# Performance work log

Measured on AMD Instinct MI355X. Metric: run time of the kernel, lower is better.

Reference implementation:

```python
import jax, jax.numpy as jnp
import numpy as np

N_NODES = 100000
N_EDGES = 1000000
IN_FEATS = 64
HID = 128
NUM_CLASSES = 10


def setup_inputs() -> dict:
    key = jax.random.key(0)
    ks = jax.random.split(key, 8)
    x = jax.random.normal(ks[0], (N_NODES, IN_FEATS), dtype=jnp.float32)
    edge_index = jax.random.randint(ks[1], (2, N_EDGES), 0, N_NODES, dtype=jnp.int64)
    # Glorot-style init scale for weights
    def w(k, fan_in, fan_out):
        s = (2.0 / (fan_in + fan_out)) ** 0.5
        return jax.random.normal(k, (fan_in, fan_out), dtype=jnp.float32) * s
    return {
        "x": x,
        "edge_index": edge_index,
        "W1": w(ks[2], IN_FEATS, HID),
        "b1": jnp.zeros((HID,), dtype=jnp.float32),
        "W2": w(ks[3], HID, HID),
        "b2": jnp.zeros((HID,), dtype=jnp.float32),
        "Wl": w(ks[4], HID, NUM_CLASSES),
        "bl": jnp.zeros((NUM_CLASSES,), dtype=jnp.float32),
    }


def _gcn_conv(x, src, dst, norm, W, b, num_nodes):
    # PyG GCNConv: h = x W, then out_i = sum_{j->i} norm_ij * h_j + b
    h = x @ W  # [N, out]
    msgs = h[src] * norm[:, None]  # gather + scale  [E+N, out]
    out = jax.ops.segment_sum(msgs, dst, num_segments=num_nodes)
    return out + b


def reference(x, edge_index, W1, b1, W2, b2, Wl, bl):
    N = x.shape[0]
    loops = jnp.arange(N, dtype=edge_index.dtype)
    src = jnp.concatenate([edge_index[0], loops])  # source nodes (messages from)
    dst = jnp.concatenate([edge_index[1], loops])  # target nodes (aggregate at)
    # symmetric normalization: deg over targets (includes self-loops)
    deg = jax.ops.segment_sum(jnp.ones(dst.shape, dtype=x.dtype), dst, num_segments=N)
    dinv = jnp.where(deg > 0, jax.lax.rsqrt(deg), 0.0)
    norm = dinv[src] * dinv[dst]  # [E+N]

    h = jax.nn.relu(_gcn_conv(x, src, dst, norm, W1, b1, N))
    h = jax.nn.relu(_gcn_conv(h, src, dst, norm, W2, b2, N))
    return jax.nn.log_softmax(h @ Wl + bl, axis=1)
```

## Files before the change

kernel.cpp:

```cpp
#include <hip/hip_runtime.h>
#include <hip/hip_fp16.h>
#include <math.h>

#define NUM_CLASSES 10

#define BSH 7
#define BSZ 128
#define BCAP 1792
#define NBMAX 1024
#define P1BATCH 4096

typedef _Float16 half8  __attribute__((ext_vector_type(8)));
typedef _Float16 half4t __attribute__((ext_vector_type(4)));
typedef float    floatx4 __attribute__((ext_vector_type(4)));

__global__ __launch_bounds__(256) void prep_kernel(const float* __restrict__ W1,
                                                   const float* __restrict__ W2,
                                                   const float* __restrict__ Wlc,
                                                   _Float16* __restrict__ W1t,
                                                   _Float16* __restrict__ W2t,
                                                   _Float16* __restrict__ Wct,
                                                   int* __restrict__ fill, int nbuck) {
    const int b = blockIdx.x, tid = threadIdx.x;
    if (b == 0) {
        for (int i = tid; i < nbuck; i += 256) fill[i] = 0;
    }
    if (b < 32) {
        int i = b * 256 + tid;
        int k = i >> 7, c = i & 127;
        W1t[c * 72 + k] = (_Float16)W1[i];
    } else if (b < 96) {
        int i = (b - 32) * 256 + tid;
        int k = i >> 7, c = i & 127;
        W2t[c * 136 + k] = (_Float16)W2[i];
    } else {
        for (int i = tid; i < 16 * 136; i += 256) {
            int c = i / 136, k = i - c * 136;
            float v = (c < NUM_CLASSES && k < 128) ? Wlc[k * NUM_CLASSES + c] : 0.0f;
            Wct[i] = (_Float16)v;
        }
    }
}

__global__ __launch_bounds__(256) void csr_p1_kernel(const int* __restrict__ src,
                                                     const int* __restrict__ dst,
                                                     int* __restrict__ bucket_fill,
                                                     unsigned* __restrict__ pairs, int E) {
    __shared__ int hist[NBMAX], base[NBMAX], cur[NBMAX];
    const int tid = threadIdx.x;
    for (int i = tid; i < NBMAX; i += 256) { hist[i] = 0; cur[i] = 0; }
    __syncthreads();
    const int bb = blockIdx.x * P1BATCH;
    unsigned pk[16];
    int bk[16];
    int cnt = 0;
#pragma unroll
    for (int i = 0; i < 16; ++i) {
        int idx = bb + i * 256 + tid;
        if (idx < E) {
            int s = src[idx], d = dst[idx];
            bk[i] = d >> BSH;
            pk[i] = ((unsigned)s << BSH) | (unsigned)(d & (BSZ - 1));
            atomicAdd(&hist[bk[i]], 1);
            cnt = i + 1;
        }
    }
    __syncthreads();
    for (int i = tid; i < NBMAX; i += 256)
        if (hist[i] > 0) base[i] = atomicAdd(&bucket_fill[i], hist[i]);
    __syncthreads();
#pragma unroll
    for (int i = 0; i < 16; ++i) {
        if (i < cnt) {
            int b = bk[i];
            int r = atomicAdd(&cur[b], 1) + base[b];
            if (r < BCAP) pairs[(size_t)b * BCAP + r] = pk[i];
        }
    }
}

__global__ __launch_bounds__(256) void scan_base_kernel(const int* __restrict__ fill,
                                                        int* __restrict__ bbase, int nbuck) {
    __shared__ int s1[256];
    const int tid = threadIdx.x;
    const int i0 = tid * 4;
    int v[4];
#pragma unroll
    for (int j = 0; j < 4; ++j) v[j] = (i0 + j < nbuck) ? fill[i0 + j] : 0;
    int t = v[0] + v[1] + v[2] + v[3];
    s1[tid] = t;
    __syncthreads();
    for (int off = 1; off < 256; off <<= 1) {
        int u = (tid >= off) ? s1[tid - off] : 0;
        __syncthreads();
        s1[tid] += u;
        __syncthreads();
    }
    int run = s1[tid] - t;
#pragma unroll
    for (int j = 0; j < 4; ++j) {
        if (i0 + j < nbuck) { bbase[i0 + j] = run; run += v[j]; }
    }
    if (tid == 255) bbase[nbuck] = s1[255];
}

__global__ __launch_bounds__(256) void csr_p2_kernel(const int* __restrict__ bucket_fill,
                                                     const int* __restrict__ bucket_base,
                                                     const unsigned* __restrict__ pairs,
                                                     const float* __restrict__ x,
                                                     int* __restrict__ rowstart,
                                                     float* __restrict__ dinv,
                                                     int* __restrict__ csr_src,
                                                     __half2* __restrict__ xs_h,
                                                     int N, int nbuck) {
    __shared__ int cnt[BSZ], excl[BSZ], cur[BSZ];
    __shared__ int s1[BSZ];
    const int tid = threadIdx.x;
    const int b = blockIdx.x;
    const int node0 = b << BSH;
    const int nodes_b = min(BSZ, N - node0);

    if (tid < BSZ) { cnt[tid] = 0; cur[tid] = 0; }
    __syncthreads();
    const int bbase = bucket_base[b];
    const int ne = bucket_fill[b];

    const unsigned* bp = pairs + (size_t)b * BCAP;
    for (int i = tid; i < ne; i += 256)
        atomicAdd(&cnt[bp[i] & (BSZ - 1)], 1);
    __syncthreads();
    int c = (tid < BSZ) ? cnt[tid] : 0;
    if (tid < BSZ) s1[tid] = c;
    __syncthreads();
    for (int off = 1; off < BSZ; off <<= 1) {
        int t = (tid < BSZ && tid >= off) ? s1[tid - off] : 0;
        __syncthreads();
        if (tid < BSZ) s1[tid] += t;
        __syncthreads();
    }
    if (tid < BSZ) excl[tid] = s1[tid] - c;
    __syncthreads();

    if (tid < nodes_b) {
        rowstart[node0 + tid] = bbase + excl[tid];
        dinv[node0 + tid] = rsqrtf((float)cnt[tid] + 1.0f);
    }
    if (b == nbuck - 1 && tid == 0) rowstart[N] = bbase + ne;

    for (int i = tid; i < nodes_b * 32; i += 256) {
        int ln = i >> 5;
        float d = rsqrtf((float)cnt[ln] + 1.0f);
        float2 v = ((const float2*)x)[(size_t)node0 * 32 + i];
        xs_h[(size_t)node0 * 32 + i] = __floats2half2_rn(v.x * d, v.y * d);
    }
    for (int i = tid; i < ne; i += 256) {
        unsigned p = bp[i];
        int d = (int)(p & (BSZ - 1));
        int r = atomicAdd(&cur[d], 1);
        csr_src[bbase + excl[d] + r] = (int)(p >> BSH);
    }
}

template <int F>
__global__ __launch_bounds__(256) void gather_h_kernel(const __half2* __restrict__ hs,
                                                       const float* __restrict__ dinv,
                                                       const int* __restrict__ rowstart,
                                                       const int* __restrict__ csr_src,
                                                       __half2* __restrict__ out, int N) {
    constexpr int F2 = F / 2;
    int node = (blockIdx.x * 256 + threadIdx.x) >> 6;
    int lane = threadIdx.x & 63;
    if (node >= N) return;
    int f2 = lane & (F2 - 1);

    int beg = rowstart[node];
    int end = rowstart[node + 1];
    int deg = end - beg;

    float2 self = __half22float2(hs[(size_t)node * F2 + f2]);
    float2 acc;

    if (deg <= 16) {
        int myidx = (lane < deg) ? csr_src[beg + lane] : node;
        float comp = (float)(deg - 15);
        acc.x = self.x * comp;
        acc.y = self.y * comp;
        float2 v[16];
#pragma unroll
        for (int u = 0; u < 16; ++u) {
            int s = __shfl(myidx, u);
            v[u] = __half22float2(hs[(size_t)s * F2 + f2]);
        }
#pragma unroll
        for (int u = 0; u < 16; ++u) { acc.x += v[u].x; acc.y += v[u].y; }
    } else {
        int lim = deg < 64 ? deg : 64;
        int myidx = (lane < lim) ? csr_src[beg + lane] : node;
        int itersUp = (lim + 7) & ~7;
        float comp = (float)(1 - (itersUp - lim));
        acc.x = self.x * comp;
        acc.y = self.y * comp;
        for (int j = 0; j < itersUp; j += 8) {
            int s[8];
#pragma unroll
            for (int u = 0; u < 8; ++u) s[u] = __shfl(myidx, j + u);
            float2 v[8];
#pragma unroll
            for (int u = 0; u < 8; ++u) v[u] = __half22float2(hs[(size_t)s[u] * F2 + f2]);
#pragma unroll
            for (int u = 0; u < 8; ++u) { acc.x += v[u].x; acc.y += v[u].y; }
        }
        for (int j = beg + 64; j < end; ++j) {
            int s = csr_src[j];
            float2 v = __half22float2(hs[(size_t)s * F2 + f2]);
            acc.x += v.x;
            acc.y += v.y;
        }
    }

    if (F == 128 || lane < 32) {
        float d = dinv[node];
        out[(size_t)node * F2 + f2] = __floats2half2_rn(d * acc.x, d * acc.y);
    }
}

template <int K, bool SCALE_OUT>
__global__ __launch_bounds__(256) void gemm_mfma_kernel(const _Float16* __restrict__ In,
                                                        const _Float16* __restrict__ Wt,
                                                        const float* __restrict__ bias,
                                                        const float* __restrict__ dinv,
                                                        _Float16* __restrict__ Out, int N) {
    constexpr int KP = K + 8;
    constexpr int NC = K / 32;
    __shared__ _Float16 Wl[128 * KP];
    __shared__ float bias_s[128];
    const int tid = threadIdx.x;

    for (int i = tid; i < (128 * KP) / 8; i += 256)
        ((floatx4*)Wl)[i] = ((const floatx4*)Wt)[i];
    if (tid < 128) bias_s[tid] = bias[tid];
    __syncthreads();

    const int lane = tid & 63;
    const int wave = tid >> 6;
    const int q = lane >> 4;
    const int l15 = lane & 15;

#pragma unroll
    for (int iter = 0; iter < 2; ++iter) {
        int myrow = blockIdx.x * 128 + iter * 64 + wave * 16 + l15;
        int r = myrow < N ? myrow : N - 1;
        half8 xf[NC];
#pragma unroll
        for (int c = 0; c < NC; ++c)
            xf[c] = *(const half8*)(In + (size_t)r * K + c * 32 + q * 8);
        floatx4 acc[8];
#pragma unroll
        for (int t = 0; t < 8; ++t) acc[t] = (floatx4){0.f, 0.f, 0.f, 0.f};
#pragma unroll
        for (int c = 0; c < NC; ++c) {
#pragma unroll
            for (int t = 0; t < 8; ++t) {
                half8 wf = *(const half8*)(Wl + (t * 16 + l15) * KP + c * 32 + q * 8);
                acc[t] = __builtin_amdgcn_mfma_f32_16x16x32_f16(wf, xf[c], acc[t], 0, 0, 0);
            }
        }
        if (myrow < N) {
            float sc = SCALE_OUT ? dinv[myrow] : 1.0f;
#pragma unroll
            for (int t = 0; t < 8; ++t) {
                int c0 = t * 16 + q * 4;
                floatx4 bv = *(const floatx4*)&bias_s[c0];
                half4t h;
#pragma unroll
                for (int j = 0; j < 4; ++j)
                    h[j] = (_Float16)(sc * fmaxf(acc[t][j] + bv[j], 0.0f));
                *(half4t*)(Out + (size_t)myrow * 128 + c0) = h;
            }
        }
    }
}

__global__ __launch_bounds__(256) void gemm_final_kernel(const _Float16* __restrict__ In,
                                                         const _Float16* __restrict__ Wt,
                                                         const float* __restrict__ bias,
                                                         const _Float16* __restrict__ Wct,
                                                         const float* __restrict__ bl,
                                                         float* __restrict__ out, int N) {
    constexpr int K = 128, KP = 136, NC = 4;
    __shared__ _Float16 Wl[128 * KP];
    __shared__ _Float16 Wc[16 * KP];
    __shared__ float bias_s[128];
    __shared__ float bl_s[16];
    __shared__ _Float16 act_s[4][16 * KP];
    const int tid = threadIdx.x;

    for (int i = tid; i < (128 * KP) / 8; i += 256)
        ((floatx4*)Wl)[i] = ((const floatx4*)Wt)[i];
    for (int i = tid; i < (16 * KP) / 8; i += 256)
        ((floatx4*)Wc)[i] = ((const floatx4*)Wct)[i];
    if (tid < 128) bias_s[tid] = bias[tid];
    if (tid < 16) bl_s[tid] = (tid < NUM_CLASSES) ? bl[tid] : -1e30f;
    __syncthreads();

    const int lane = tid & 63;
    const int wave = tid >> 6;
    const int q = lane >> 4;
    const int l15 = lane & 15;
    _Float16* As = act_s[wave];

    half8 wcf[NC];
#pragma unroll
    for (int c = 0; c < NC; ++c)
        wcf[c] = *(const half8*)(Wc + l15 * KP + c * 32 + q * 8);
    float myclsb[4];
#pragma unroll
    for (int reg = 0; reg < 4; ++reg) myclsb[reg] = bl_s[q * 4 + reg];

#pragma unroll
    for (int iter = 0; iter < 2; ++iter) {
        int rowbase = blockIdx.x * 128 + iter * 64 + wave * 16;
        int myrow = rowbase + l15;
        int r = myrow < N ? myrow : N - 1;
        half8 xf[NC];
#pragma unroll
        for (int c = 0; c < NC; ++c)
            xf[c] = *(const half8*)(In + (size_t)r * K + c * 32 + q * 8);
        floatx4 acc[8];
#pragma unroll
        for (int t = 0; t < 8; ++t) acc[t] = (floatx4){0.f, 0.f, 0.f, 0.f};
#pragma unroll
        for (int c = 0; c < NC; ++c) {
#pragma unroll
            for (int t = 0; t < 8; ++t) {
                half8 wf = *(const half8*)(Wl + (t * 16 + l15) * KP + c * 32 + q * 8);
                acc[t] = __builtin_amdgcn_mfma_f32_16x16x32_f16(wf, xf[c], acc[t], 0, 0, 0);
            }
        }
#pragma unroll
        for (int t = 0; t < 8; ++t) {
            int c0 = t * 16 + q * 4;
            floatx4 bv = *(const floatx4*)&bias_s[c0];
            half4t h;
#pragma unroll
            for (int j = 0; j < 4; ++j)
                h[j] = (_Float16)fmaxf(acc[t][j] + bv[j], 0.0f);
            *(half4t*)&As[l15 * KP + c0] = h;
        }
        floatx4 lg = (floatx4){0.f, 0.f, 0.f, 0.f};
#pragma unroll
        for (int c = 0; c < NC; ++c) {
            half8 af = *(const half8*)(As + l15 * KP + c * 32 + q * 8);
            lg = __builtin_amdgcn_mfma_f32_16x16x32_f16(wcf[c], af, lg, 0, 0, 0);
        }
        if (myrow < N) {
            float v[4];
#pragma unroll
            for (int reg = 0; reg < 4; ++reg) v[reg] = lg[reg] + myclsb[reg];
            float mx = fmaxf(fmaxf(v[0], v[1]), fmaxf(v[2], v[3]));
            mx = fmaxf(mx, __shfl_xor(mx, 16));
            mx = fmaxf(mx, __shfl_xor(mx, 32));
            float sm = expf(v[0] - mx) + expf(v[1] - mx) + expf(v[2] - mx) + expf(v[3] - mx);
            sm += __shfl_xor(sm, 16);
            sm += __shfl_xor(sm, 32);
            float lse = mx + logf(sm);
#pragma unroll
            for (int reg = 0; reg < 4; ++reg) {
                int cls = q * 4 + reg;
                if (cls < NUM_CLASSES)
                    out[(size_t)myrow * NUM_CLASSES + cls] = v[reg] - lse;
            }
        }
    }
}

extern "C" void kernel_launch(void* const* d_in, const int* in_sizes, int n_in,
                              void* d_out, int out_size, void* d_ws, size_t ws_size,
                              hipStream_t stream) {
    const float* x  = (const float*)d_in[0];
    const int*   ei = (const int*)d_in[1];
    const float* W1 = (const float*)d_in[2];
    const float* b1 = (const float*)d_in[3];
    const float* W2 = (const float*)d_in[4];
    const float* b2 = (const float*)d_in[5];
    const float* Wlc = (const float*)d_in[6];
    const float* bl = (const float*)d_in[7];
    float* out = (float*)d_out;

    const int N = in_sizes[0] / 64;
    const int E = in_sizes[1] / 2;
    const int* src = ei;
    const int* dst = ei + E;
    const int nbuck = (N + BSZ - 1) >> BSH;

    char* ws = (char*)d_ws;
    int*      bucket_fill = (int*)(ws + 0);
    int*      rowstart    = (int*)(ws + 4096);
    float*    dinv        = (float*)(ws + 524288);
    _Float16* W1t         = (_Float16*)(ws + 1048576);
    _Float16* W2t         = (_Float16*)(ws + 1069056);
    _Float16* Wct         = (_Float16*)(ws + 1103872);
    int*      bucket_base = (int*)(ws + 1110016);
    unsigned* pairs       = (unsigned*)(ws + 2097152);
    int*      csr_src     = (int*)(ws + 12582912);
    char*     region1     = ws + 16777216;
    char*     region2     = ws + 68157440;
    __half2*  xs_h = (__half2*)region1;
    __half2*  g1h  = (__half2*)(region1 + 13631488);
    __half2*  g2h  = (__half2*)region1;
    __half2*  a1_h = (__half2*)region2;

    const int P1B = (E + P1BATCH - 1) / P1BATCH;
    const int GB  = (N + 127) / 128;
    const int WVB = (N + 3) / 4;

    prep_kernel<<<97, 256, 0, stream>>>(W1, W2, Wlc, W1t, W2t, Wct, bucket_fill, nbuck);
    csr_p1_kernel<<<P1B, 256, 0, stream>>>(src, dst, bucket_fill, pairs, E);
    scan_base_kernel<<<1, 256, 0, stream>>>(bucket_fill, bucket_base, nbuck);
    csr_p2_kernel<<<nbuck, 256, 0, stream>>>(bucket_fill, bucket_base, pairs, x, rowstart,
                                             dinv, csr_src, xs_h, N, nbuck);

    gather_h_kernel<64><<<WVB, 256, 0, stream>>>(xs_h, dinv, rowstart, csr_src, g1h, N);
    gemm_mfma_kernel<64, true><<<GB, 256, 0, stream>>>((const _Float16*)g1h, W1t, b1, dinv,
                                                       (_Float16*)a1_h, N);

    gather_h_kernel<128><<<WVB, 256, 0, stream>>>(a1_h, dinv, rowstart, csr_src, g2h, N);
    gemm_final_kernel<<<GB, 256, 0, stream>>>((const _Float16*)g2h, W2t, b2, Wct, bl, out, N);
}
```

Measured before the change: 226.0 us.

## Fuse prep into CSR pass, drop scan kernel, split gathers by feature width

Merges the weight-conversion prep kernel into the CSR bucketing pass and zeroes the bucket counts with an async memset. The first pass now stages its pairs in shared memory, sorted by bucket, so the global writes come out contiguous. The separate single-block scan kernel is removed, and each csr_p2 block instead reduces the preceding bucket counts itself. The 64-feature gather now uses both half-waves, each taking alternate neighbours, and combines the two halves with a cross-lane shuffle. Together these aim to cut launch count and idle lanes, at the cost of redundant prefix sums in every p2 block and more shared memory per block in the first pass.

Result: slower. 233.0 us (+3.1%).

```diff
diff --git a/kernel.cpp b/kernel.cpp
--- a/kernel.cpp
+++ b/kernel.cpp
@@ -9,48 +9,57 @@
 #define BCAP 1792
 #define NBMAX 1024
 #define P1BATCH 4096
+#define PREPB 97
 
 typedef _Float16 half8  __attribute__((ext_vector_type(8)));
 typedef _Float16 half4t __attribute__((ext_vector_type(4)));
 typedef float    floatx4 __attribute__((ext_vector_type(4)));
 
-__global__ __launch_bounds__(256) void prep_kernel(const float* __restrict__ W1,
-                                                   const float* __restrict__ W2,
-                                                   const float* __restrict__ Wlc,
-                                                   _Float16* __restrict__ W1t,
-                                                   _Float16* __restrict__ W2t,
-                                                   _Float16* __restrict__ Wct,
-                                                   int* __restrict__ fill, int nbuck) {
-    const int b = blockIdx.x, tid = threadIdx.x;
-    if (b == 0) {
-        for (int i = tid; i < nbuck; i += 256) fill[i] = 0;
-    }
-    if (b < 32) {
-        int i = b * 256 + tid;
-        int k = i >> 7, c = i & 127;
-        W1t[c * 72 + k] = (_Float16)W1[i];
-    } else if (b < 96) {
-        int i = (b - 32) * 256 + tid;
-        int k = i >> 7, c = i & 127;
-        W2t[c * 136 + k] = (_Float16)W2[i];
-    } else {
-        for (int i = tid; i < 16 * 136; i += 256) {
-            int c = i / 136, k = i - c * 136;
-            float v = (c < NUM_CLASSES && k < 128) ? Wlc[k * NUM_CLASSES + c] : 0.0f;
-            Wct[i] = (_Float16)v;
-        }
-    }
-}
-
-__global__ __launch_bounds__(256) void csr_p1_kernel(const int* __restrict__ src,
-                                                     const int* __restrict__ dst,
-                                                     int* __restrict__ bucket_fill,
-                                                     unsigned* __restrict__ pairs, int E) {
-    __shared__ int hist[NBMAX], base[NBMAX], cur[NBMAX];
+__global__ __launch_bounds__(256) void prep_p1_kernel(const float* __restrict__ W1,
+                                                      const float* __restrict__ W2,
+                                                      const float* __restrict__ Wlc,
+                                                      _Float16* __restrict__ W1t,
+                                                      _Float16* __restrict__ W2t,
+                                                      _Float16* __restrict__ Wct,
+                                                      const int* __restrict__ src,
+                                                      const int* __restrict__ dst,
+                                                      int* __restrict__ bucket_fill,
+                                                      unsigned* __restrict__ pairs, int E) {
+    __shared__ int hist[NBMAX];
+    __shared__ int lofs[NBMAX];
+    __shared__ int gbase[NBMAX];
+    __shared__ int cur[NBMAX];
+    __shared__ int s1[256];
+    __shared__ unsigned stage[P1BATCH];
+    __shared__ unsigned short sbk[P1BATCH];
     const int tid = threadIdx.x;
+    const int b = blockIdx.x;
+
+    if (b < PREPB) {
+        if (b < 32) {
+            int i = b * 256 + tid;
+            int k = i >> 7, c = i & 127;
+            W1t[c * 72 + k] = (_Float16)W1[i];
+        } else if (b < 96) {
+            int i = (b - 32) * 256 + tid;
+            int k = i >> 7, c = i & 127;
+            W2t[c * 136 + k] = (_Float16)W2[i];
+        } else {
+            for (int i = tid; i < 16 * 136; i += 256) {
+                int c = i / 136, k = i - c * 136;
+                float v = (c < NUM_CLASSES && k < 128) ? Wlc[k * NUM_CLASSES + c] : 0.0f;
+                Wct[i] = (_Float16)v;
+            }
+        }
+        return;
+    }
+
+    const int blk = b - PREPB;
     for (int i = tid; i < NBMAX; i += 256) { hist[i] = 0; cur[i] = 0; }
     __syncthreads();
-    const int bb = blockIdx.x * P1BATCH;
+
+    const int bb = blk * P1BATCH;
+    const int bcnt = min(P1BATCH, E - bb);
     unsigned pk[16];
     int bk[16];
     int cnt = 0;
@@ -66,46 +75,45 @@
         }
     }
     __syncthreads();
-    for (int i = tid; i < NBMAX; i += 256)
-        if (hist[i] > 0) base[i] = atomicAdd(&bucket_fill[i], hist[i]);
+    const int i0 = tid * 4;
+    int h4[4];
+    int ssum = 0;
+#pragma unroll
+    for (int j = 0; j < 4; ++j) { h4[j] = hist[i0 + j]; ssum += h4[j]; }
+    s1[tid] = ssum;
+    __syncthreads();
+    for (int off = 1; off < 256; off <<= 1) {
+        int t = (tid >= off) ? s1[tid - off] : 0;
+        __syncthreads();
+        s1[tid] += t;
+        __syncthreads();
+    }
+    int run = s1[tid] - ssum;
+#pragma unroll
+    for (int j = 0; j < 4; ++j) { lofs[i0 + j] = run; run += h4[j]; }
+#pragma unroll
+    for (int j = 0; j < 4; ++j)
+        gbase[i0 + j] = (h4[j] > 0) ? atomicAdd(&bucket_fill[i0 + j], h4[j]) : 0;
     __syncthreads();
 #pragma unroll
     for (int i = 0; i < 16; ++i) {
         if (i < cnt) {
-            int b = bk[i];
-            int r = atomicAdd(&cur[b], 1) + base[b];
-            if (r < BCAP) pairs[(size_t)b * BCAP + r] = pk[i];
-        }
-    }
-}
-
-__global__ __launch_bounds__(256) void scan_base_kernel(const int* __restrict__ fill,
-                                                        int* __restrict__ bbase, int nbuck) {
-    __shared__ int s1[256];
-    const int tid = threadIdx.x;
-    const int i0 = tid * 4;
-    int v[4];
-#pragma unroll
-    for (int j = 0; j < 4; ++j) v[j] = (i0 + j < nbuck) ? fill[i0 + j] : 0;
-    int t = v[0] + v[1] + v[2] + v[3];
-    s1[tid] = t;
-    __syncthreads();
-    for (int off = 1; off < 256; off <<= 1) {
-        int u = (tid >= off) ? s1[tid - off] : 0;
-        __syncthreads();
-        s1[tid] += u;
-        __syncthreads();
-    }
-    int run = s1[tid] - t;
-#pragma unroll
-    for (int j = 0; j < 4; ++j) {
-        if (i0 + j < nbuck) { bbase[i0 + j] = run; run += v[j]; }
-    }
-    if (tid == 255) bbase[nbuck] = s1[255];
+            int bi = bk[i];
+            int r = atomicAdd(&cur[bi], 1);
+            int slot = lofs[bi] + r;
+            stage[slot] = pk[i];
+            sbk[slot] = (unsigned short)bi;
+        }
+    }
+    __syncthreads();
+    for (int j = tid; j < bcnt; j += 256) {
+        int bi = sbk[j];
+        int g = gbase[bi] + (j - lofs[bi]);
+        if (g < BCAP) pairs[(size_t)bi * BCAP + g] = stage[j];
+    }
 }
 
 __global__ __launch_bounds__(256) void csr_p2_kernel(const int* __restrict__ bucket_fill,
-                                                     const int* __restrict__ bucket_base,
                                                      const unsigned* __restrict__ pairs,
                                                      const float* __restrict__ x,
                                                      int* __restrict__ rowstart,
@@ -114,16 +122,24 @@
                                                      __half2* __restrict__ xs_h,
                                                      int N, int nbuck) {
     __shared__ int cnt[BSZ], excl[BSZ], cur[BSZ];
-    __shared__ int s1[BSZ];
+    __shared__ int s1[256];
     const int tid = threadIdx.x;
     const int b = blockIdx.x;
     const int node0 = b << BSH;
     const int nodes_b = min(BSZ, N - node0);
 
     if (tid < BSZ) { cnt[tid] = 0; cur[tid] = 0; }
-    __syncthreads();
-    const int bbase = bucket_base[b];
+    int part = 0;
+    for (int j = tid; j < b; j += 256) part += bucket_fill[j];
+    s1[tid] = part;
+    __syncthreads();
+    for (int off = 128; off > 0; off >>= 1) {
+        if (tid < off) s1[tid] += s1[tid + off];
+        __syncthreads();
+    }
+    const int bbase = s1[0];
     const int ne = bucket_fill[b];
+    __syncthreads();
 
     const unsigned* bp = pairs + (size_t)b * BCAP;
     for (int i = tid; i < ne; i += 256)
@@ -161,67 +177,113 @@
     }
 }
 
-template <int F>
-__global__ __launch_bounds__(256) void gather_h_kernel(const __half2* __restrict__ hs,
+__global__ __launch_bounds__(256) void gather64_kernel(const __half2* __restrict__ xs,
                                                        const float* __restrict__ dinv,
                                                        const int* __restrict__ rowstart,
                                                        const int* __restrict__ csr_src,
                                                        __half2* __restrict__ out, int N) {
-    constexpr int F2 = F / 2;
     int node = (blockIdx.x * 256 + threadIdx.x) >> 6;
     int lane = threadIdx.x & 63;
     if (node >= N) return;
-    int f2 = lane & (F2 - 1);
+    const int h = lane >> 5;
+    const int f2 = lane & 31;
 
     int beg = rowstart[node];
     int end = rowstart[node + 1];
     int deg = end - beg;
 
-    float2 self = __half22float2(hs[(size_t)node * F2 + f2]);
-    float2 acc;
+    float2 self = __half22float2(xs[(size_t)node * 32 + f2]);
+    float2 acc = make_float2(0.f, 0.f);
 
     if (deg <= 16) {
         int myidx = (lane < deg) ? csr_src[beg + lane] : node;
-        float comp = (float)(deg - 15);
-        acc.x = self.x * comp;
-        acc.y = self.y * comp;
-        float2 v[16];
-#pragma unroll
-        for (int u = 0; u < 16; ++u) {
-            int s = __shfl(myidx, u);
-            v[u] = __half22float2(hs[(size_t)s * F2 + f2]);
-        }
-#pragma unroll
-        for (int u = 0; u < 16; ++u) { acc.x += v[u].x; acc.y += v[u].y; }
+        if (h == 0) {
+            float cmp = (float)(deg - 15);
+            acc.x = self.x * cmp;
+            acc.y = self.y * cmp;
+        }
+        float2 v[8];
+#pragma unroll
+        for (int u = 0; u < 8; ++u) {
+            int s = __shfl(myidx, 2 * u + h);
+            v[u] = __half22float2(xs[(size_t)s * 32 + f2]);
+        }
+#pragma unroll
+        for (int u = 0; u < 8; ++u) { acc.x += v[u].x; acc.y += v[u].y; }
     } else {
         int lim = deg < 64 ? deg : 64;
         int myidx = (lane < lim) ? csr_src[beg + lane] : node;
-        int itersUp = (lim + 7) & ~7;
-        float comp = (float)(1 - (itersUp - lim));
-        acc.x = self.x * comp;
-        acc.y = self.y * comp;
-        for (int j = 0; j < itersUp; j += 8) {
-            int s[8];
-#pragma unroll
-            for (int u = 0; u < 8; ++u) s[u] = __shfl(myidx, j + u);
+        int itersUp = (lim + 15) & ~15;
+        if (h == 0) {
+            float cmp = (float)(1 - (itersUp - lim));
+            acc.x = self.x * cmp;
+            acc.y = self.y * cmp;
+        }
+        for (int j = 0; j < itersUp; j += 16) {
             float2 v[8];
 #pragma unroll
-            for (int u = 0; u < 8; ++u) v[u] = __half22float2(hs[(size_t)s[u] * F2 + f2]);
+            for (int u = 0; u < 8; ++u) {
+                int s = __shfl(myidx, j + 2 * u + h);
+                v[u] = __half22float2(xs[(size_t)s * 32 + f2]);
+            }
 #pragma unroll
             for (int u = 0; u < 8; ++u) { acc.x += v[u].x; acc.y += v[u].y; }
         }
-        for (int j = beg + 64; j < end; ++j) {
-            int s = csr_src[j];
-            float2 v = __half22float2(hs[(size_t)s * F2 + f2]);
-            acc.x += v.x;
-            acc.y += v.y;
-        }
-    }
-
-    if (F == 128 || lane < 32) {
+        if (h == 0) {
+            for (int j = beg + 64; j < end; ++j) {
+                float2 v = __half22float2(xs[(size_t)csr_src[j] * 32 + f2]);
+                acc.x += v.x;
+                acc.y += v.y;
+            }
+        }
+    }
+    acc.x += __shfl_xor(acc.x, 32);
+    acc.y += __shfl_xor(acc.y, 32);
+    if (lane < 32) {
         float d = dinv[node];
-        out[(size_t)node * F2 + f2] = __floats2half2_rn(d * acc.x, d * acc.y);
-    }
+        out[(size_t)node * 32 + f2] = __floats2half2_rn(d * acc.x, d * acc.y);
+    }
+}
+
+__global__ __launch_bounds__(256) void gather128_kernel(const __half2* __restrict__ hs,
+                                                        const float* __restrict__ dinv,
+                                                        const int* __restrict__ rowstart,
+                                                        const int* __restrict__ csr_src,
+                                                        __half2* __restrict__ out, int N) {
+    int node = (blockIdx.x * 256 + threadIdx.x) >> 6;
+    int lane = threadIdx.x & 63;
+    if (node >= N) return;
+
+    int beg = rowstart[node];
+    int end = rowstart[node + 1];
+    int deg = end - beg;
+
+    float2 self = __half22float2(hs[(size_t)node * 64 + lane]);
+    int lim = deg < 64 ? deg : 64;
+    int myidx = (lane < lim) ? csr_src[beg + lane] : node;
+    int itersUp = (lim + 7) & ~7;
+    float comp = (float)(1 - (itersUp - lim));
+    float2 acc;
+    acc.x = self.x * comp;
+    acc.y = self.y * comp;
+
+    for (int j = 0; j < itersUp; j += 8) {
+        int s[8];
+#pragma unroll
+        for (int u = 0; u < 8; ++u) s[u] = __shfl(myidx, j + u);
+        float2 v[8];
+#pragma unroll
+        for (int u = 0; u < 8; ++u) v[u] = __half22float2(hs[(size_t)s[u] * 64 + lane]);
+#pragma unroll
+        for (int u = 0; u < 8; ++u) { acc.x += v[u].x; acc.y += v[u].y; }
+    }
+    for (int j = beg + 64; j < end; ++j) {
+        float2 v = __half22float2(hs[(size_t)csr_src[j] * 64 + lane]);
+        acc.x += v.x;
+        acc.y += v.y;
+    }
+    float d = dinv[node];
+    out[(size_t)node * 64 + lane] = __floats2half2_rn(d * acc.x, d * acc.y);
 }
 
 template <int K, bool SCALE_OUT>
@@ -271,11 +333,11 @@
             for (int t = 0; t < 8; ++t) {
                 int c0 = t * 16 + q * 4;
                 floatx4 bv = *(const floatx4*)&bias_s[c0];
-                half4t h;
+                half4t hh;
 #pragma unroll
                 for (int j = 0; j < 4; ++j)
-                    h[j] = (_Float16)(sc * fmaxf(acc[t][j] + bv[j], 0.0f));
-                *(half4t*)(Out + (size_t)myrow * 128 + c0) = h;
+                    hh[j] = (_Float16)(sc * fmaxf(acc[t][j] + bv[j], 0.0f));
+                *(half4t*)(Out + (size_t)myrow * 128 + c0) = hh;
             }
         }
     }
@@ -319,8 +381,7 @@
 
 #pragma unroll
     for (int iter = 0; iter < 2; ++iter) {
-        int rowbase = blockIdx.x * 128 + iter * 64 + wave * 16;
-        int myrow = rowbase + l15;
+        int myrow = blockIdx.x * 128 + iter * 64 + wave * 16 + l15;
         int r = myrow < N ? myrow : N - 1;
         half8 xf[NC];
 #pragma unroll
@@ -341,11 +402,11 @@
         for (int t = 0; t < 8; ++t) {
             int c0 = t * 16 + q * 4;
             floatx4 bv = *(const floatx4*)&bias_s[c0];
-            half4t h;
+            half4t hh;
 #pragma unroll
             for (int j = 0; j < 4; ++j)
-                h[j] = (_Float16)fmaxf(acc[t][j] + bv[j], 0.0f);
-            *(half4t*)&As[l15 * KP + c0] = h;
+                hh[j] = (_Float16)fmaxf(acc[t][j] + bv[j], 0.0f);
+            *(half4t*)&As[l15 * KP + c0] = hh;
         }
         floatx4 lg = (floatx4){0.f, 0.f, 0.f, 0.f};
 #pragma unroll
@@ -400,30 +461,27 @@
     _Float16* W1t         = (_Float16*)(ws + 1048576);
     _Float16* W2t         = (_Float16*)(ws + 1069056);
     _Float16* Wct         = (_Float16*)(ws + 1103872);
-    int*      bucket_base = (int*)(ws + 1110016);
     unsigned* pairs       = (unsigned*)(ws + 2097152);
     int*      csr_src     = (int*)(ws + 12582912);
-    char*     region1     = ws + 16777216;
-    char*     region2     = ws + 68157440;
-    __half2*  xs_h = (__half2*)region1;
-    __half2*  g1h  = (__half2*)(region1 + 13631488);
-    __half2*  g2h  = (__half2*)region1;
-    __half2*  a1_h = (__half2*)region2;
+    __half2*  xs_h        = (__half2*)(ws + 16777216);
+    __half2*  g1h         = (__half2*)(ws + 33554432);
+    __half2*  g2h         = (__half2*)(ws + 46923776);
+    __half2*  a1_h        = (__half2*)(ws + 73400320);
 
     const int P1B = (E + P1BATCH - 1) / P1BATCH;
     const int GB  = (N + 127) / 128;
     const int WVB = (N + 3) / 4;
 
-    prep_kernel<<<97, 256, 0, stream>>>(W1, W2, Wlc, W1t, W2t, Wct, bucket_fill, nbuck);
-    csr_p1_kernel<<<P1B, 256, 0, stream>>>(src, dst, bucket_fill, pairs, E);
-    scan_base_kernel<<<1, 256, 0, stream>>>(bucket_fill, bucket_base, nbuck);
-    csr_p2_kernel<<<nbuck, 256, 0, stream>>>(bucket_fill, bucket_base, pairs, x, rowstart,
-                                             dinv, csr_src, xs_h, N, nbuck);
-
-    gather_h_kernel<64><<<WVB, 256, 0, stream>>>(xs_h, dinv, rowstart, csr_src, g1h, N);
+    hipMemsetAsync(bucket_fill, 0, nbuck * sizeof(int), stream);
+    prep_p1_kernel<<<PREPB + P1B, 256, 0, stream>>>(W1, W2, Wlc, W1t, W2t, Wct,
+                                                    src, dst, bucket_fill, pairs, E);
+    csr_p2_kernel<<<nbuck, 256, 0, stream>>>(bucket_fill, pairs, x, rowstart, dinv,
+                                             csr_src, xs_h, N, nbuck);
+
+    gather64_kernel<<<WVB, 256, 0, stream>>>(xs_h, dinv, rowstart, csr_src, g1h, N);
     gemm_mfma_kernel<64, true><<<GB, 256, 0, stream>>>((const _Float16*)g1h, W1t, b1, dinv,
                                                        (_Float16*)a1_h, N);
 
-    gather_h_kernel<128><<<WVB, 256, 0, stream>>>(a1_h, dinv, rowstart, csr_src, g2h, N);
+    gather128_kernel<<<WVB, 256, 0, stream>>>(a1_h, dinv, rowstart, csr_src, g2h, N);
     gemm_final_kernel<<<GB, 256, 0, stream>>>((const _Float16*)g2h, W2t, b2, Wct, bl, out, N);
 }
```
